# Optimization experiments

Measured on AMD Instinct MI355X. Metric: run time of the kernel, lower is better.

The kernel has to match this reference:

```python
import jax, jax.numpy as jnp
import numpy as np

HEADS = 8
DHEAD = 64
A_SCALE = 8.0  # cosine-attention logit scale (a=8 in source)
ROPE_BASE = 10000.0


def _mp_weight(w, centered):
    # Magnitude-preserving (EDM2-style) weight: optional zero-mean over fan-in,
    # unit-norm per output row, scaled by 1/sqrt(fan_in).
    if centered:
        w = w - w.mean(axis=1, keepdims=True)
    w = w / (jnp.linalg.norm(w, axis=1, keepdims=True) + 1e-8)
    return w / jnp.sqrt(jnp.asarray(w.shape[1], w.dtype))


def _rope_cos_sin(Hs, Ws, d, dtype=jnp.float32):
    # 2D axial RoPE: first d/4 rotation pairs encode row position, last d/4 column position.
    quarter = d // 4
    freqs = 1.0 / (ROPE_BASE ** (jnp.arange(quarter, dtype=dtype) / quarter))  # [d/4]
    ah = jnp.arange(Hs, dtype=dtype)[:, None] * freqs                          # [H, d/4]
    aw = jnp.arange(Ws, dtype=dtype)[:, None] * freqs                          # [W, d/4]
    ang = jnp.concatenate([
        jnp.broadcast_to(ah[:, None, :], (Hs, Ws, quarter)),
        jnp.broadcast_to(aw[None, :, :], (Hs, Ws, quarter)),
    ], axis=-1).reshape(Hs * Ws, d // 2)                                       # [L, d/2]
    return jnp.cos(ang), jnp.sin(ang)


def _apply_rope(t, cos, sin):
    # t: [N, h, L, d]; rotate interleaved pairs.
    x1, x2 = t[..., 0::2], t[..., 1::2]
    r1 = x1 * cos - x2 * sin
    r2 = x1 * sin + x2 * cos
    return jnp.stack([r1, r2], axis=-1).reshape(t.shape)


def setup_inputs() -> dict:
    key = jax.random.key(0)
    ks = jax.random.split(key, 8)
    N, C, Hs, Ws = 8, 256, 32, 32
    E, Hc = 512, 512
    return {
        "x": jax.random.normal(ks[0], (N, C, Hs, Ws), jnp.float32),
        "w": jax.random.normal(ks[1], (N, E), jnp.float32),
        "InputGain": jax.random.uniform(ks[2], (3 * Hc,), jnp.float32),
        "ResidualGain": jax.random.uniform(ks[3], (C,), jnp.float32),
        "qkv_w": jax.random.normal(ks[4], (3 * Hc, C), jnp.float32),
        "qkv_b": jnp.zeros((3 * Hc,), jnp.float32),
        "mod_w": jax.random.normal(ks[5], (E, C), jnp.float32) / jnp.sqrt(512.0),
        "proj_w": jax.random.normal(ks[6], (C, Hc), jnp.float32),
        "sinks": jnp.zeros((HEADS,), jnp.float32),
    }


def reference(x, w, InputGain, ResidualGain, qkv_w, qkv_b, mod_w, proj_w, sinks):
    N, C, Hs, Ws = x.shape
    L = Hs * Ws
    Hc = qkv_w.shape[0] // 3

    # --- fused QKV: style-modulated, biased, centered 1x1 conv with per-out-channel gain ---
    style = w @ mod_w + 1.0                                   # [N, C]
    Wq = _mp_weight(qkv_w, centered=True)                     # [3Hc, C]
    xm = x * style[:, :, None, None]
    y = jnp.einsum('nchw,oc->nohw', xm, Wq)
    y = (y + qkv_b[None, :, None, None]) * InputGain[None, :, None, None]  # [N, 3Hc, H, W]

    # --- split heads, flatten space: [N, h, L, d] ---
    y = y.reshape(N, 3, HEADS, DHEAD, L)
    q = jnp.transpose(y[:, 0], (0, 1, 3, 2))
    k = jnp.transpose(y[:, 1], (0, 1, 3, 2))
    v = jnp.transpose(y[:, 2], (0, 1, 3, 2))

    # --- 2D RoPE on q, k ---
    cos, sin = _rope_cos_sin(Hs, Ws, DHEAD, x.dtype)
    q = _apply_rope(q, cos, sin)
    k = _apply_rope(k, cos, sin)

    # --- cosine attention with per-head sink logit ---
    qn = q / (jnp.linalg.norm(q, axis=-1, keepdims=True) + 1e-8)
    kn = k / (jnp.linalg.norm(k, axis=-1, keepdims=True) + 1e-8)
    logits = A_SCALE * jnp.einsum('nhld,nhmd->nhlm', qn, kn)  # [N, h, L, L]
    sink = jnp.broadcast_to(sinks[None, :, None, None], (N, HEADS, L, 1))
    probs = jax.nn.softmax(jnp.concatenate([logits, sink], axis=-1), axis=-1)[..., :L]
    o = jnp.einsum('nhlm,nhmd->nhld', probs, v)               # [N, h, L, d]

    # --- merge heads back to map, centered 1x1 projection with per-out-channel gain ---
    o = jnp.transpose(o, (0, 1, 3, 2)).reshape(N, Hc, Hs, Ws)
    Wp = _mp_weight(proj_w, centered=True) * ResidualGain[:, None]  # [C, Hc]
    out = jnp.einsum('nchw,oc->nohw', o, Wp)
    return x + out
```

## Files before the change

### kernel.cpp

```cpp
#include <hip/hip_runtime.h>
#include <hip/hip_bf16.h>
#include <math.h>

#define NN 8
#define CC 256
#define LL 1024
#define EE 512
#define HEADS 8
#define DH 64

#define OFF_STYLE   0u
#define OFF_BIAS    2048u
#define OFF_COS     3584u
#define OFF_SIN     36352u
#define OFF_WQB     69120u
#define OFF_WPB     265728u
#define OFF_XMT     331264u
#define OFF_Q       1379840u
#define OFF_K       3476992u
#define OFF_V       5574144u
#define OFF_O       7671296u

typedef __bf16 bf16x8 __attribute__((ext_vector_type(8)));
typedef __bf16 bf16x4 __attribute__((ext_vector_type(4)));
typedef short s16x4 __attribute__((ext_vector_type(4)));
typedef short s16x8 __attribute__((ext_vector_type(8)));
typedef float f32x4 __attribute__((ext_vector_type(4)));

__global__ __launch_bounds__(256) void k_prep(
    const float* __restrict__ w, const float* __restrict__ mod_w, float* __restrict__ style,
    const float* __restrict__ qkv_w, const float* __restrict__ gain,
    const float* __restrict__ bias, __hip_bfloat16* __restrict__ wqb, float* __restrict__ biasg,
    const float* __restrict__ proj_w, const float* __restrict__ rgain,
    __hip_bfloat16* __restrict__ wpb,
    float* __restrict__ cosT, float* __restrict__ sinT) {
    int bid = blockIdx.x;
    int t = threadIdx.x;
    int wv = t >> 6, lane = t & 63;
    if (bid < 384) {
        int o = bid * 4 + wv;
        float4 v = *reinterpret_cast<const float4*>(qkv_w + o * CC + lane * 4);
        float s = v.x + v.y + v.z + v.w;
        #pragma unroll
        for (int off = 1; off < 64; off <<= 1) s += __shfl_xor(s, off);
        float mean = s * (1.0f / 256.0f);
        float c0 = v.x - mean, c1 = v.y - mean, c2 = v.z - mean, c3 = v.w - mean;
        float ss = c0 * c0 + c1 * c1 + c2 * c2 + c3 * c3;
        #pragma unroll
        for (int off = 1; off < 64; off <<= 1) ss += __shfl_xor(ss, off);
        float g = gain[o];
        float scale = g / ((sqrtf(ss) + 1e-8f) * 16.0f);
        bf16x4 outv;
        outv[0] = (__bf16)(c0 * scale); outv[1] = (__bf16)(c1 * scale);
        outv[2] = (__bf16)(c2 * scale); outv[3] = (__bf16)(c3 * scale);
        *reinterpret_cast<bf16x4*>((__bf16*)wqb + o * CC + lane * 4) = outv;
        if (lane == 0) biasg[o] = bias[o] * g;
    } else if (bid < 448) {
        int r = (bid - 384) * 4 + wv;
        const float* p = proj_w + r * 512 + lane * 8;
        float4 v0 = *reinterpret_cast<const float4*>(p);
        float4 v1 = *reinterpret_cast<const float4*>(p + 4);
        float s = v0.x + v0.y + v0.z + v0.w + v1.x + v1.y + v1.z + v1.w;
        #pragma unroll
        for (int off = 1; off < 64; off <<= 1) s += __shfl_xor(s, off);
        float mean = s * (1.0f / 512.0f);
        float c[8] = {v0.x - mean, v0.y - mean, v0.z - mean, v0.w - mean,
                      v1.x - mean, v1.y - mean, v1.z - mean, v1.w - mean};
        float ss = 0.f;
        #pragma unroll
        for (int i = 0; i < 8; ++i) ss += c[i] * c[i];
        #pragma unroll
        for (int off = 1; off < 64; off <<= 1) ss += __shfl_xor(ss, off);
        float scale = rgain[r] / ((sqrtf(ss) + 1e-8f) * 22.62741699796952f);
        bf16x8 outv;
        #pragma unroll
        for (int i = 0; i < 8; ++i) outv[i] = (__bf16)(c[i] * scale);
        *reinterpret_cast<bf16x8*>((__bf16*)wpb + r * 512 + lane * 8) = outv;
    } else if (bid < 512) {
        int idx = (bid - 448) * 256 + t;
        int l = idx >> 4, j = idx & 15;
        int hh = l >> 5, ww = l & 31;
        float f = exp2f(-(float)j * 0.8304820238941836f);
        float s1, c1, s2, c2;
        __sincosf((float)hh * f, &s1, &c1);
        __sincosf((float)ww * f, &s2, &c2);
        cosT[l * 32 + j]      = c1;
        sinT[l * 32 + j]      = s1;
        cosT[l * 32 + 16 + j] = c2;
        sinT[l * 32 + 16 + j] = s2;
    } else {
        int b = bid - 512;
        int n = b >> 2, cg = b & 3;
        int c = cg * 64 + lane;
        __shared__ float red[4][64];
        float acc = 0.f;
        #pragma unroll 8
        for (int e = wv * 128; e < wv * 128 + 128; ++e)
            acc += w[n * EE + e] * mod_w[e * CC + c];
        red[wv][lane] = acc;
        __syncthreads();
        if (wv == 0)
            style[n * CC + c] = red[0][lane] + red[1][lane] + red[2][lane] + red[3][lane] + 1.0f;
    }
}

__global__ __launch_bounds__(256) void k_xm(const float* __restrict__ x,
                                            const float* __restrict__ style,
                                            __hip_bfloat16* __restrict__ xmT) {
    int lb = blockIdx.x;
    int cb = blockIdx.y;
    int n  = blockIdx.z;
    int t = threadIdx.x;
    __shared__ float tile[64][68];
    int r = t >> 2, q = t & 3;
    float st = style[n * CC + cb * 64 + r];
    const float* xp = x + (size_t)n * (CC * LL) + (size_t)(cb * 64 + r) * LL + lb * 64 + q * 16;
    #pragma unroll
    for (int i = 0; i < 4; ++i) {
        float4 v = *reinterpret_cast<const float4*>(xp + i * 4);
        tile[r][q * 16 + i * 4 + 0] = v.x * st;
        tile[r][q * 16 + i * 4 + 1] = v.y * st;
        tile[r][q * 16 + i * 4 + 2] = v.z * st;
        tile[r][q * 16 + i * 4 + 3] = v.w * st;
    }
    __syncthreads();
    __hip_bfloat16 outv[16];
    #pragma unroll
    for (int i = 0; i < 16; ++i)
        outv[i] = __float2bfloat16(tile[q * 16 + i][r]);
    __hip_bfloat16* dst = xmT + (size_t)n * (LL * CC) + (size_t)(lb * 64 + r) * CC + cb * 64 + q * 16;
    *reinterpret_cast<bf16x8*>(dst)     = *reinterpret_cast<bf16x8*>(&outv[0]);
    *reinterpret_cast<bf16x8*>(dst + 8) = *reinterpret_cast<bf16x8*>(&outv[8]);
}

__global__ __launch_bounds__(256) void k_qkv3(const __hip_bfloat16* __restrict__ wqb,
                                              const __hip_bfloat16* __restrict__ xmT,
                                              const float* __restrict__ biasg,
                                              const float* __restrict__ cosT,
                                              const float* __restrict__ sinT,
                                              __hip_bfloat16* __restrict__ qb,
                                              __hip_bfloat16* __restrict__ kb,
                                              __hip_bfloat16* __restrict__ vt) {
    int lb = blockIdx.x;
    int ob = blockIdx.y;
    int n  = blockIdx.z;
    int tid = threadIdx.x;
    int wid = tid >> 6, lane = tid & 63;
    int wr = wid >> 1, wc = wid & 1;
    int g = lane >> 4, r16 = lane & 15;

    int o0 = ob * 128 + wr * 64;
    int l0 = lb * 128 + wc * 64;
    int part = o0 >> 9;
    int h = (o0 & 511) >> 6;

    __shared__ __hip_bfloat16 smem[32768];

    const int srow[4] = {tid >> 3, (tid + 256) >> 3, (tid + 512) >> 3, (tid + 768) >> 3};
    const int scol = (tid & 7) * 8;
    int sswz[4];
    #pragma unroll
    for (int i = 0; i < 4; ++i) sswz[i] = scol ^ ((srow[i] & 7) << 3);

    const __hip_bfloat16* Agl = wqb + (size_t)(ob * 128) * CC;
    const __hip_bfloat16* Bgl = xmT + (size_t)n * (LL * CC) + (size_t)(lb * 128) * CC;

    bf16x8 ar[4], br[4];
    #pragma unroll
    for (int i = 0; i < 4; ++i) {
        ar[i] = *reinterpret_cast<const bf16x8*>(Agl + (size_t)srow[i] * CC + scol);
        br[i] = *reinterpret_cast<const bf16x8*>(Bgl + (size_t)srow[i] * CC + scol);
    }
    #pragma unroll
    for (int i = 0; i < 4; ++i) {
        *reinterpret_cast<bf16x8*>(&smem[srow[i] * 64 + sswz[i]]) = ar[i];
        *reinterpret_cast<bf16x8*>(&smem[16384 + srow[i] * 64 + sswz[i]]) = br[i];
    }
    __syncthreads();

    f32x4 acc[4][4] = {};
    int cur = 0;
    for (int t = 0; t < 4; ++t) {
        if (t < 3) {
            int kt1 = (t + 1) * 64;
            #pragma unroll
            for (int i = 0; i < 4; ++i) {
                ar[i] = *reinterpret_cast<const bf16x8*>(Agl + (size_t)srow[i] * CC + kt1 + scol);
                br[i] = *reinterpret_cast<const bf16x8*>(Bgl + (size_t)srow[i] * CC + kt1 + scol);
            }
        }
        const __hip_bfloat16* At = &smem[cur * 8192];
        const __hip_bfloat16* Bt = &smem[16384 + cur * 8192];
        #pragma unroll
        for (int kk = 0; kk < 2; ++kk) {
            int col = (kk * 32 + g * 8) ^ ((r16 & 7) << 3);
            bf16x8 a[4], b[4];
            #pragma unroll
            for (int m = 0; m < 4; ++m)
                a[m] = *reinterpret_cast<const bf16x8*>(&At[(wr * 64 + m * 16 + r16) * 64 + col]);
            #pragma unroll
            for (int nn = 0; nn < 4; ++nn)
                b[nn] = *reinterpret_cast<const bf16x8*>(&Bt[(wc * 64 + nn * 16 + r16) * 64 + col]);
            __builtin_amdgcn_s_setprio(1);
            #pragma unroll
            for (int m = 0; m < 4; ++m)
                #pragma unroll
                for (int nn = 0; nn < 4; ++nn)
                    acc[m][nn] = __builtin_amdgcn_mfma_f32_16x16x32_bf16(a[m], b[nn], acc[m][nn], 0, 0, 0);
            __builtin_amdgcn_s_setprio(0);
        }
        if (t < 3) {
            #pragma unroll
            for (int i = 0; i < 4; ++i) {
                *reinterpret_cast<bf16x8*>(&smem[(cur ^ 1) * 8192 + srow[i] * 64 + sswz[i]]) = ar[i];
                *reinterpret_cast<bf16x8*>(&smem[16384 + (cur ^ 1) * 8192 + srow[i] * 64 + sswz[i]]) = br[i];
            }
        }
        __syncthreads();
        cur ^= 1;
    }

    __hip_bfloat16 (*sw)[64][72] = reinterpret_cast<__hip_bfloat16 (*)[64][72]>(smem);

    float bg[4][4];
    #pragma unroll
    for (int m = 0; m < 4; ++m)
        #pragma unroll
        for (int reg = 0; reg < 4; ++reg)
            bg[m][reg] = biasg[o0 + m * 16 + 4 * g + reg];

    size_t head = (size_t)(n * 8 + h);

    if (part < 2) {
        __hip_bfloat16* dst = (part == 0) ? qb : kb;
        #pragma unroll
        for (int nn = 0; nn < 4; ++nn) {
            int l = l0 + nn * 16 + r16;
            float rv[4][4];
            float ss = 0.f;
            #pragma unroll
            for (int m = 0; m < 4; ++m) {
                int j0 = m * 8 + g * 2;
                float cA = cosT[l * 32 + j0],     sA = sinT[l * 32 + j0];
                float cB = cosT[l * 32 + j0 + 1], sB = sinT[l * 32 + j0 + 1];
                float x0 = acc[m][nn][0] + bg[m][0];
                float x1 = acc[m][nn][1] + bg[m][1];
                float x2 = acc[m][nn][2] + bg[m][2];
                float x3 = acc[m][nn][3] + bg[m][3];
                rv[m][0] = x0 * cA - x1 * sA;
                rv[m][1] = x0 * sA + x1 * cA;
                rv[m][2] = x2 * cB - x3 * sB;
                rv[m][3] = x2 * sB + x3 * cB;
                ss += rv[m][0] * rv[m][0] + rv[m][1] * rv[m][1] +
                      rv[m][2] * rv[m][2] + rv[m][3] * rv[m][3];
            }
            ss += __shfl_xor(ss, 16);
            ss += __shfl_xor(ss, 32);
            float inv = 1.0f / (sqrtf(ss) + 1e-8f);
            #pragma unroll
            for (int m = 0; m < 4; ++m)
                #pragma unroll
                for (int reg = 0; reg < 4; ++reg)
                    sw[wid][nn * 16 + r16][m * 16 + 4 * g + reg] =
                        __float2bfloat16(rv[m][reg] * inv);
        }
        #pragma unroll
        for (int it = 0; it < 8; ++it) {
            int idx = lane + it * 64;
            int ll = idx >> 3, ch = idx & 7;
            bf16x8 v = *reinterpret_cast<bf16x8*>(&sw[wid][ll][ch * 8]);
            *reinterpret_cast<bf16x8*>(dst + (head * LL + l0 + ll) * DH + ch * 8) = v;
        }
    } else {
        #pragma unroll
        for (int nn = 0; nn < 4; ++nn)
            #pragma unroll
            for (int m = 0; m < 4; ++m)
                #pragma unroll
                for (int reg = 0; reg < 4; ++reg)
                    sw[wid][m * 16 + 4 * g + reg][nn * 16 + r16] =
                        __float2bfloat16(acc[m][nn][reg] + bg[m][reg]);
        #pragma unroll
        for (int it = 0; it < 8; ++it) {
            int idx = lane + it * 64;
            int dd = idx >> 3, ch = idx & 7;
            bf16x8 v = *reinterpret_cast<bf16x8*>(&sw[wid][dd][ch * 8]);
            *reinterpret_cast<bf16x8*>(vt + (head * DH + dd) * LL + l0 + ch * 8) = v;
        }
    }
}

__global__ __launch_bounds__(256) void k_attn_mfma(
    const __hip_bfloat16* __restrict__ qb, const __hip_bfloat16* __restrict__ kb,
    const __hip_bfloat16* __restrict__ vt, const float* __restrict__ sinks,
    __hip_bfloat16* __restrict__ ob) {
    int bid = blockIdx.x;
    int swz = (bid & 7) * 64 + (bid >> 3);
    int n    = swz >> 6;
    int h    = (swz >> 3) & 7;
    int qblk = swz & 7;
    int tid  = threadIdx.x;
    int wid  = tid >> 6, lane = tid & 63;
    int g = lane >> 4, r16 = lane & 15;

    size_t head = (size_t)(n * 8 + h);
    const __hip_bfloat16* Q = qb + head * (size_t)(LL * DH);
    const __hip_bfloat16* K = kb + head * (size_t)(LL * DH);
    const __hip_bfloat16* V = vt + head * (size_t)(DH * LL);
    __hip_bfloat16* O = ob + (size_t)n * (LL * 512) + h * 64;

    int q0 = qblk * 128 + wid * 32;

    __shared__ __hip_bfloat16 kls[2][64][64];
    __shared__ __hip_bfloat16 vls[2][64][64];

    const int cl0 = tid >> 3,         cd0 = (tid & 7) * 8;
    const int cl1 = (tid + 256) >> 3;
    const int ksw0 = cd0 ^ ((cl0 & 7) << 3);
    const int ksw1 = cd0 ^ ((cl1 & 7) << 3);
    const int vswA0 = cd0       ^ ((cl0 & 15) << 2);
    const int vswB0 = (cd0 + 4) ^ ((cl0 & 15) << 2);
    const int vswA1 = cd0       ^ ((cl1 & 15) << 2);
    const int vswB1 = (cd0 + 4) ^ ((cl1 & 15) << 2);

    bf16x8 qf[2][2];
    #pragma unroll
    for (int qm = 0; qm < 2; ++qm)
        #pragma unroll
        for (int dc = 0; dc < 2; ++dc)
            qf[qm][dc] = *reinterpret_cast<const bf16x8*>(
                Q + (size_t)(q0 + qm * 16 + r16) * DH + dc * 32 + g * 8);

    float snk = sinks[h];
    float m = fmaxf(8.0f, snk);
    const float c1 = 8.0f * 1.44269504f;
    const float c0 = -m * 1.44269504f;

    f32x4 oacc[2][4];
    #pragma unroll
    for (int qm = 0; qm < 2; ++qm)
        #pragma unroll
        for (int dn = 0; dn < 4; ++dn)
            oacc[qm][dn] = (f32x4){0.f, 0.f, 0.f, 0.f};
    f32x4 osum[2];
    osum[0] = (f32x4){0.f, 0.f, 0.f, 0.f};
    osum[1] = (f32x4){0.f, 0.f, 0.f, 0.f};
    const s16x4 ones = {(short)0x3F80, (short)0x3F80, (short)0x3F80, (short)0x3F80};

    bf16x8 kr0, kr1, vr0, vr1;
    kr0 = *reinterpret_cast<const bf16x8*>(K + (size_t)cl0 * DH + cd0);
    kr1 = *reinterpret_cast<const bf16x8*>(K + (size_t)cl1 * DH + cd0);
    vr0 = *reinterpret_cast<const bf16x8*>(V + (size_t)cl0 * LL + cd0);
    vr1 = *reinterpret_cast<const bf16x8*>(V + (size_t)cl1 * LL + cd0);
    {
        *reinterpret_cast<bf16x8*>(&kls[0][cl0][ksw0]) = kr0;
        *reinterpret_cast<bf16x8*>(&kls[0][cl1][ksw1]) = kr1;
        s16x8 w0 = __builtin_bit_cast(s16x8, vr0);
        s16x8 w1 = __builtin_bit_cast(s16x8, vr1);
        *reinterpret_cast<s16x4*>(&vls[0][cl0][vswA0]) = __builtin_shufflevector(w0, w0, 0, 1, 2, 3);
        *reinterpret_cast<s16x4*>(&vls[0][cl0][vswB0]) = __builtin_shufflevector(w0, w0, 4, 5, 6, 7);
        *reinterpret_cast<s16x4*>(&vls[0][cl1][vswA1]) = __builtin_shufflevector(w1, w1, 0, 1, 2, 3);
        *reinterpret_cast<s16x4*>(&vls[0][cl1][vswB1]) = __builtin_shufflevector(w1, w1, 4, 5, 6, 7);
    }
    __syncthreads();

    int cur = 0;
    for (int t = 0; t < 16; ++t) {
        if (t < 15) {
            int kt1 = t * 64 + 64;
            kr0 = *reinterpret_cast<const bf16x8*>(K + (size_t)(kt1 + cl0) * DH + cd0);
            kr1 = *reinterpret_cast<const bf16x8*>(K + (size_t)(kt1 + cl1) * DH + cd0);
            vr0 = *reinterpret_cast<const bf16x8*>(V + (size_t)cl0 * LL + kt1 + cd0);
            vr1 = *reinterpret_cast<const bf16x8*>(V + (size_t)cl1 * LL + kt1 + cd0);
        }
        f32x4 sacc[2][4];
        #pragma unroll
        for (int qm = 0; qm < 2; ++qm)
            #pragma unroll
            for (int kn = 0; kn < 4; ++kn)
                sacc[qm][kn] = (f32x4){0.f, 0.f, 0.f, 0.f};
        __builtin_amdgcn_s_setprio(1);
        #pragma unroll
        for (int kn = 0; kn < 4; ++kn) {
            #pragma unroll
            for (int dc = 0; dc < 2; ++dc) {
                bf16x8 kf = *reinterpret_cast<const bf16x8*>(
                    &kls[cur][kn * 16 + r16][(dc * 32 + g * 8) ^ ((r16 & 7) << 3)]);
                #pragma unroll
                for (int qm = 0; qm < 2; ++qm)
                    sacc[qm][kn] = __builtin_amdgcn_mfma_f32_16x16x32_bf16(
                        kf, qf[qm][dc], sacc[qm][kn], 0, 0, 0);
            }
        }
        __builtin_amdgcn_s_setprio(0);
        #pragma unroll
        for (int kn = 0; kn < 4; ++kn) {
            s16x4 pa[2];
            #pragma unroll
            for (int qm = 0; qm < 2; ++qm) {
                float p0 = exp2f(fmaf(sacc[qm][kn][0], c1, c0));
                float p1 = exp2f(fmaf(sacc[qm][kn][1], c1, c0));
                float p2 = exp2f(fmaf(sacc[qm][kn][2], c1, c0));
                float p3 = exp2f(fmaf(sacc[qm][kn][3], c1, c0));
                bf16x4 pb;
                pb[0] = (__bf16)p0; pb[1] = (__bf16)p1;
                pb[2] = (__bf16)p2; pb[3] = (__bf16)p3;
                pa[qm] = __builtin_bit_cast(s16x4, pb);
            }
            __builtin_amdgcn_s_setprio(1);
            #pragma unroll
            for (int qm = 0; qm < 2; ++qm)
                osum[qm] = __builtin_amdgcn_mfma_f32_16x16x16bf16_1k(pa[qm], ones, osum[qm], 0, 0, 0);
            #pragma unroll
            for (int dn = 0; dn < 4; ++dn) {
                s16x4 vb = *reinterpret_cast<const s16x4*>(
                    &vls[cur][dn * 16 + r16][(kn * 16 + g * 4) ^ ((r16 & 15) << 2)]);
                #pragma unroll
                for (int qm = 0; qm < 2; ++qm)
                    oacc[qm][dn] = __builtin_amdgcn_mfma_f32_16x16x16bf16_1k(
                        pa[qm], vb, oacc[qm][dn], 0, 0, 0);
            }
            __builtin_amdgcn_s_setprio(0);
        }
        if (t < 15) {
            *reinterpret_cast<bf16x8*>(&kls[cur ^ 1][cl0][ksw0]) = kr0;
            *reinterpret_cast<bf16x8*>(&kls[cur ^ 1][cl1][ksw1]) = kr1;
            s16x8 w0 = __builtin_bit_cast(s16x8, vr0);
            s16x8 w1 = __builtin_bit_cast(s16x8, vr1);
            *reinterpret_cast<s16x4*>(&vls[cur ^ 1][cl0][vswA0]) = __builtin_shufflevector(w0, w0, 0, 1, 2, 3);
            *reinterpret_cast<s16x4*>(&vls[cur ^ 1][cl0][vswB0]) = __builtin_shufflevector(w0, w0, 4, 5, 6, 7);
            *reinterpret_cast<s16x4*>(&vls[cur ^ 1][cl1][vswA1]) = __builtin_shufflevector(w1, w1, 0, 1, 2, 3);
            *reinterpret_cast<s16x4*>(&vls[cur ^ 1][cl1][vswB1]) = __builtin_shufflevector(w1, w1, 4, 5, 6, 7);
        }
        __syncthreads();
        cur ^= 1;
    }

    float sink_e = exp2f((snk - m) * 1.44269504f);
    #pragma unroll
    for (int qm = 0; qm < 2; ++qm) {
        #pragma unroll
        for (int reg = 0; reg < 4; ++reg) {
            float invq = 1.0f / (osum[qm][reg] + sink_e);
            #pragma unroll
            for (int dn = 0; dn < 4; ++dn)
                O[(size_t)(q0 + qm * 16 + 4 * g + reg) * 512 + dn * 16 + r16] =
                    __float2bfloat16(oacc[qm][dn][reg] * invq);
        }
    }
}

__global__ __launch_bounds__(256) void k_proj3(const __hip_bfloat16* __restrict__ wpb,
                                               const __hip_bfloat16* __restrict__ ob,
                                               const float* __restrict__ x,
                                               float* __restrict__ out) {
    int lb = blockIdx.x;
    int cb = blockIdx.y;
    int n  = blockIdx.z;
    int tid = threadIdx.x;
    int wid = tid >> 6, lane = tid & 63;
    int wr = wid >> 1, wc = wid & 1;
    int g = lane >> 4, r16 = lane & 15;

    int c0 = cb * 64 + wr * 32;
    int l0 = lb * 128 + wc * 64;

    __shared__ __hip_bfloat16 smem[24576];

    const int arow[2] = {tid >> 3, (tid + 256) >> 3};
    const int brow[4] = {tid >> 3, (tid + 256) >> 3, (tid + 512) >> 3, (tid + 768) >> 3};
    const int scol = (tid & 7) * 8;
    int aswz[2], bswz[4];
    #pragma unroll
    for (int i = 0; i < 2; ++i) aswz[i] = scol ^ ((arow[i] & 7) << 3);
    #pragma unroll
    for (int i = 0; i < 4; ++i) bswz[i] = scol ^ ((brow[i] & 7) << 3);

    const __hip_bfloat16* Agl = wpb + (size_t)(cb * 64) * 512;
    const __hip_bfloat16* Bgl = ob + (size_t)n * (LL * 512) + (size_t)(lb * 128) * 512;

    bf16x8 ar[2], br[4];
    #pragma unroll
    for (int i = 0; i < 2; ++i)
        ar[i] = *reinterpret_cast<const bf16x8*>(Agl + (size_t)arow[i] * 512 + scol);
    #pragma unroll
    for (int i = 0; i < 4; ++i)
        br[i] = *reinterpret_cast<const bf16x8*>(Bgl + (size_t)brow[i] * 512 + scol);
    #pragma unroll
    for (int i = 0; i < 2; ++i)
        *reinterpret_cast<bf16x8*>(&smem[arow[i] * 64 + aswz[i]]) = ar[i];
    #pragma unroll
    for (int i = 0; i < 4; ++i)
        *reinterpret_cast<bf16x8*>(&smem[8192 + brow[i] * 64 + bswz[i]]) = br[i];
    __syncthreads();

    f32x4 acc[2][4] = {};
    int cur = 0;
    for (int t = 0; t < 8; ++t) {
        if (t < 7) {
            int kt1 = (t + 1) * 64;
            #pragma unroll
            for (int i = 0; i < 2; ++i)
                ar[i] = *reinterpret_cast<const bf16x8*>(Agl + (size_t)arow[i] * 512 + kt1 + scol);
            #pragma unroll
            for (int i = 0; i < 4; ++i)
                br[i] = *reinterpret_cast<const bf16x8*>(Bgl + (size_t)brow[i] * 512 + kt1 + scol);
        }
        const __hip_bfloat16* At = &smem[cur * 4096];
        const __hip_bfloat16* Bt = &smem[8192 + cur * 8192];
        #pragma unroll
        for (int kk = 0; kk < 2; ++kk) {
            int col = (kk * 32 + g * 8) ^ ((r16 & 7) << 3);
            bf16x8 a[2], b[4];
            #pragma unroll
            for (int m = 0; m < 2; ++m)
                a[m] = *reinterpret_cast<const bf16x8*>(&At[(wr * 32 + m * 16 + r16) * 64 + col]);
            #pragma unroll
            for (int nn = 0; nn < 4; ++nn)
                b[nn] = *reinterpret_cast<const bf16x8*>(&Bt[(wc * 64 + nn * 16 + r16) * 64 + col]);
            __builtin_amdgcn_s_setprio(1);
            #pragma unroll
            for (int m = 0; m < 2; ++m)
                #pragma unroll
                for (int nn = 0; nn < 4; ++nn)
                    acc[m][nn] = __builtin_amdgcn_mfma_f32_16x16x32_bf16(a[m], b[nn], acc[m][nn], 0, 0, 0);
            __builtin_amdgcn_s_setprio(0);
        }
        if (t < 7) {
            #pragma unroll
            for (int i = 0; i < 2; ++i)
                *reinterpret_cast<bf16x8*>(&smem[(cur ^ 1) * 4096 + arow[i] * 64 + aswz[i]]) = ar[i];
            #pragma unroll
            for (int i = 0; i < 4; ++i)
                *reinterpret_cast<bf16x8*>(&smem[8192 + (cur ^ 1) * 8192 + brow[i] * 64 + bswz[i]]) = br[i];
        }
        __syncthreads();
        cur ^= 1;
    }

    #pragma unroll
    for (int m = 0; m < 2; ++m) {
        #pragma unroll
        for (int reg = 0; reg < 4; ++reg) {
            int c = c0 + m * 16 + 4 * g + reg;
            #pragma unroll
            for (int nn = 0; nn < 4; ++nn) {
                int l = l0 + nn * 16 + r16;
                size_t idx = (size_t)n * (CC * LL) + (size_t)c * LL + l;
                out[idx] = x[idx] + acc[m][nn][reg];
            }
        }
    }
}

extern "C" void kernel_launch(void* const* d_in, const int* in_sizes, int n_in,
                              void* d_out, int out_size, void* d_ws, size_t ws_size,
                              hipStream_t stream) {
    const float* x       = (const float*)d_in[0];
    const float* w       = (const float*)d_in[1];
    const float* igain   = (const float*)d_in[2];
    const float* rgain   = (const float*)d_in[3];
    const float* qkv_w   = (const float*)d_in[4];
    const float* qkv_b   = (const float*)d_in[5];
    const float* mod_w   = (const float*)d_in[6];
    const float* proj_w  = (const float*)d_in[7];
    const float* sinks   = (const float*)d_in[8];
    float* out = (float*)d_out;
    float* ws  = (float*)d_ws;

    float* style = ws + OFF_STYLE;
    float* biasg = ws + OFF_BIAS;
    float* cosT  = ws + OFF_COS;
    float* sinT  = ws + OFF_SIN;
    __hip_bfloat16* wqb = (__hip_bfloat16*)(ws + OFF_WQB);
    __hip_bfloat16* wpb = (__hip_bfloat16*)(ws + OFF_WPB);
    __hip_bfloat16* xmT = (__hip_bfloat16*)(ws + OFF_XMT);
    __hip_bfloat16* qb  = (__hip_bfloat16*)(ws + OFF_Q);
    __hip_bfloat16* kb  = (__hip_bfloat16*)(ws + OFF_K);
    __hip_bfloat16* vt  = (__hip_bfloat16*)(ws + OFF_V);
    __hip_bfloat16* obuf = (__hip_bfloat16*)(ws + OFF_O);

    k_prep<<<544, 256, 0, stream>>>(w, mod_w, style, qkv_w, igain, qkv_b, wqb, biasg,
                                    proj_w, rgain, wpb, cosT, sinT);
    k_xm<<<dim3(16, 4, NN), 256, 0, stream>>>(x, style, xmT);
    k_qkv3<<<dim3(8, 12, NN), 256, 0, stream>>>(wqb, xmT, biasg, cosT, sinT, qb, kb, vt);
    k_attn_mfma<<<512, 256, 0, stream>>>(qb, kb, vt, sinks, obuf);
    k_proj3<<<dim3(8, 4, NN), 256, 0, stream>>>(wpb, obuf, x, out);
}
```

Before: 83.63 us.

## Fold softmax scale into Q and widen attention K/V tiles to 128

The cosine-attention logit scale (8·log2e) is folded into the Q normalization in the QKV kernel, so the attention loop feeds raw scores straight into exp2f. This drops the fixed max-subtraction, which is safe because scores are bounded, and the sink term is adjusted to match. The attention kernel now stages 128-key K/V tiles per iteration (8 iterations instead of 16), halving barriers and global-load rounds. The cost is double the shared memory per block and more staging registers, which may lower occupancy.

Result: faster. 81.91 us (-2.1%).

```diff
diff --git a/kernel.cpp b/kernel.cpp
--- a/kernel.cpp
+++ b/kernel.cpp
@@ -233,6 +233,7 @@
 
     if (part < 2) {
         __hip_bfloat16* dst = (part == 0) ? qb : kb;
+        float qscale = (part == 0) ? 11.541560327111707f : 1.0f;
         #pragma unroll
         for (int nn = 0; nn < 4; ++nn) {
             int l = l0 + nn * 16 + r16;
@@ -256,7 +257,7 @@
             }
             ss += __shfl_xor(ss, 16);
             ss += __shfl_xor(ss, 32);
-            float inv = 1.0f / (sqrtf(ss) + 1e-8f);
+            float inv = qscale / (sqrtf(ss) + 1e-8f);
             #pragma unroll
             for (int m = 0; m < 4; ++m)
                 #pragma unroll
@@ -311,17 +312,18 @@
 
     int q0 = qblk * 128 + wid * 32;
 
-    __shared__ __hip_bfloat16 kls[2][64][64];
-    __shared__ __hip_bfloat16 vls[2][64][64];
-
-    const int cl0 = tid >> 3,         cd0 = (tid & 7) * 8;
-    const int cl1 = (tid + 256) >> 3;
-    const int ksw0 = cd0 ^ ((cl0 & 7) << 3);
-    const int ksw1 = cd0 ^ ((cl1 & 7) << 3);
-    const int vswA0 = cd0       ^ ((cl0 & 15) << 2);
-    const int vswB0 = (cd0 + 4) ^ ((cl0 & 15) << 2);
-    const int vswA1 = cd0       ^ ((cl1 & 15) << 2);
-    const int vswB1 = (cd0 + 4) ^ ((cl1 & 15) << 2);
+    __shared__ __hip_bfloat16 kls[2][128][64];
+    __shared__ __hip_bfloat16 vls[2][64][128];
+
+    const int kcl = tid >> 3, kcd = (tid & 7) * 8;
+    const int vcl = tid >> 4, vcd = (tid & 15) * 8;
+    int kswz[4], vswzA[4], vswzB[4];
+    #pragma unroll
+    for (int i = 0; i < 4; ++i) {
+        kswz[i]  = kcd ^ (((kcl + i * 32) & 7) << 3);
+        vswzA[i] = vcd ^ (((vcl + i * 16) & 15) << 2);
+        vswzB[i] = (vcd + 4) ^ (((vcl + i * 16) & 15) << 2);
+    }
 
     bf16x8 qf[2][2];
     #pragma unroll
@@ -332,9 +334,6 @@
                 Q + (size_t)(q0 + qm * 16 + r16) * DH + dc * 32 + g * 8);
 
     float snk = sinks[h];
-    float m = fmaxf(8.0f, snk);
-    const float c1 = 8.0f * 1.44269504f;
-    const float c0 = -m * 1.44269504f;
 
     f32x4 oacc[2][4];
     #pragma unroll
@@ -347,96 +346,99 @@
     osum[1] = (f32x4){0.f, 0.f, 0.f, 0.f};
     const s16x4 ones = {(short)0x3F80, (short)0x3F80, (short)0x3F80, (short)0x3F80};
 
-    bf16x8 kr0, kr1, vr0, vr1;
-    kr0 = *reinterpret_cast<const bf16x8*>(K + (size_t)cl0 * DH + cd0);
-    kr1 = *reinterpret_cast<const bf16x8*>(K + (size_t)cl1 * DH + cd0);
-    vr0 = *reinterpret_cast<const bf16x8*>(V + (size_t)cl0 * LL + cd0);
-    vr1 = *reinterpret_cast<const bf16x8*>(V + (size_t)cl1 * LL + cd0);
-    {
-        *reinterpret_cast<bf16x8*>(&kls[0][cl0][ksw0]) = kr0;
-        *reinterpret_cast<bf16x8*>(&kls[0][cl1][ksw1]) = kr1;
-        s16x8 w0 = __builtin_bit_cast(s16x8, vr0);
-        s16x8 w1 = __builtin_bit_cast(s16x8, vr1);
-        *reinterpret_cast<s16x4*>(&vls[0][cl0][vswA0]) = __builtin_shufflevector(w0, w0, 0, 1, 2, 3);
-        *reinterpret_cast<s16x4*>(&vls[0][cl0][vswB0]) = __builtin_shufflevector(w0, w0, 4, 5, 6, 7);
-        *reinterpret_cast<s16x4*>(&vls[0][cl1][vswA1]) = __builtin_shufflevector(w1, w1, 0, 1, 2, 3);
-        *reinterpret_cast<s16x4*>(&vls[0][cl1][vswB1]) = __builtin_shufflevector(w1, w1, 4, 5, 6, 7);
+    bf16x8 kr[4], vr[4];
+    #pragma unroll
+    for (int i = 0; i < 4; ++i) {
+        kr[i] = *reinterpret_cast<const bf16x8*>(K + (size_t)(kcl + i * 32) * DH + kcd);
+        vr[i] = *reinterpret_cast<const bf16x8*>(V + (size_t)(vcl + i * 16) * LL + vcd);
+    }
+    #pragma unroll
+    for (int i = 0; i < 4; ++i) {
+        *reinterpret_cast<bf16x8*>(&kls[0][kcl + i * 32][kswz[i]]) = kr[i];
+        s16x8 wv8 = __builtin_bit_cast(s16x8, vr[i]);
+        *reinterpret_cast<s16x4*>(&vls[0][vcl + i * 16][vswzA[i]]) = __builtin_shufflevector(wv8, wv8, 0, 1, 2, 3);
+        *reinterpret_cast<s16x4*>(&vls[0][vcl + i * 16][vswzB[i]]) = __builtin_shufflevector(wv8, wv8, 4, 5, 6, 7);
     }
     __syncthreads();
 
     int cur = 0;
-    for (int t = 0; t < 16; ++t) {
-        if (t < 15) {
-            int kt1 = t * 64 + 64;
-            kr0 = *reinterpret_cast<const bf16x8*>(K + (size_t)(kt1 + cl0) * DH + cd0);
-            kr1 = *reinterpret_cast<const bf16x8*>(K + (size_t)(kt1 + cl1) * DH + cd0);
-            vr0 = *reinterpret_cast<const bf16x8*>(V + (size_t)cl0 * LL + kt1 + cd0);
-            vr1 = *reinterpret_cast<const bf16x8*>(V + (size_t)cl1 * LL + kt1 + cd0);
-        }
-        f32x4 sacc[2][4];
-        #pragma unroll
-        for (int qm = 0; qm < 2; ++qm)
-            #pragma unroll
-            for (int kn = 0; kn < 4; ++kn)
-                sacc[qm][kn] = (f32x4){0.f, 0.f, 0.f, 0.f};
-        __builtin_amdgcn_s_setprio(1);
-        #pragma unroll
-        for (int kn = 0; kn < 4; ++kn) {
-            #pragma unroll
-            for (int dc = 0; dc < 2; ++dc) {
-                bf16x8 kf = *reinterpret_cast<const bf16x8*>(
-                    &kls[cur][kn * 16 + r16][(dc * 32 + g * 8) ^ ((r16 & 7) << 3)]);
+    for (int t = 0; t < 8; ++t) {
+        if (t < 7) {
+            int kt1 = (t + 1) * 128;
+            #pragma unroll
+            for (int i = 0; i < 4; ++i) {
+                kr[i] = *reinterpret_cast<const bf16x8*>(K + (size_t)(kt1 + kcl + i * 32) * DH + kcd);
+                vr[i] = *reinterpret_cast<const bf16x8*>(V + (size_t)(vcl + i * 16) * LL + kt1 + vcd);
+            }
+        }
+        #pragma unroll
+        for (int sub = 0; sub < 2; ++sub) {
+            f32x4 sacc[2][4];
+            #pragma unroll
+            for (int qm = 0; qm < 2; ++qm)
+                #pragma unroll
+                for (int kn = 0; kn < 4; ++kn)
+                    sacc[qm][kn] = (f32x4){0.f, 0.f, 0.f, 0.f};
+            __builtin_amdgcn_s_setprio(1);
+            #pragma unroll
+            for (int kn = 0; kn < 4; ++kn) {
+                int krow = sub * 64 + kn * 16 + r16;
+                #pragma unroll
+                for (int dc = 0; dc < 2; ++dc) {
+                    bf16x8 kf = *reinterpret_cast<const bf16x8*>(
+                        &kls[cur][krow][(dc * 32 + g * 8) ^ ((r16 & 7) << 3)]);
+                    #pragma unroll
+                    for (int qm = 0; qm < 2; ++qm)
+                        sacc[qm][kn] = __builtin_amdgcn_mfma_f32_16x16x32_bf16(
+                            kf, qf[qm][dc], sacc[qm][kn], 0, 0, 0);
+                }
+            }
+            __builtin_amdgcn_s_setprio(0);
+            #pragma unroll
+            for (int kn = 0; kn < 4; ++kn) {
+                s16x4 pa[2];
+                #pragma unroll
+                for (int qm = 0; qm < 2; ++qm) {
+                    float p0 = exp2f(sacc[qm][kn][0]);
+                    float p1 = exp2f(sacc[qm][kn][1]);
+                    float p2 = exp2f(sacc[qm][kn][2]);
+                    float p3 = exp2f(sacc[qm][kn][3]);
+                    bf16x4 pb;
+                    pb[0] = (__bf16)p0; pb[1] = (__bf16)p1;
+                    pb[2] = (__bf16)p2; pb[3] = (__bf16)p3;
+                    pa[qm] = __builtin_bit_cast(s16x4, pb);
+                }
+                __builtin_amdgcn_s_setprio(1);
                 #pragma unroll
                 for (int qm = 0; qm < 2; ++qm)
-                    sacc[qm][kn] = __builtin_amdgcn_mfma_f32_16x16x32_bf16(
-                        kf, qf[qm][dc], sacc[qm][kn], 0, 0, 0);
-            }
-        }
-        __builtin_amdgcn_s_setprio(0);
-        #pragma unroll
-        for (int kn = 0; kn < 4; ++kn) {
-            s16x4 pa[2];
-            #pragma unroll
-            for (int qm = 0; qm < 2; ++qm) {
-                float p0 = exp2f(fmaf(sacc[qm][kn][0], c1, c0));
-                float p1 = exp2f(fmaf(sacc[qm][kn][1], c1, c0));
-                float p2 = exp2f(fmaf(sacc[qm][kn][2], c1, c0));
-                float p3 = exp2f(fmaf(sacc[qm][kn][3], c1, c0));
-                bf16x4 pb;
-                pb[0] = (__bf16)p0; pb[1] = (__bf16)p1;
-                pb[2] = (__bf16)p2; pb[3] = (__bf16)p3;
-                pa[qm] = __builtin_bit_cast(s16x4, pb);
-            }
-            __builtin_amdgcn_s_setprio(1);
-            #pragma unroll
-            for (int qm = 0; qm < 2; ++qm)
-                osum[qm] = __builtin_amdgcn_mfma_f32_16x16x16bf16_1k(pa[qm], ones, osum[qm], 0, 0, 0);
-            #pragma unroll
-            for (int dn = 0; dn < 4; ++dn) {
-                s16x4 vb = *reinterpret_cast<const s16x4*>(
-                    &vls[cur][dn * 16 + r16][(kn * 16 + g * 4) ^ ((r16 & 15) << 2)]);
-                #pragma unroll
-                for (int qm = 0; qm < 2; ++qm)
-                    oacc[qm][dn] = __builtin_amdgcn_mfma_f32_16x16x16bf16_1k(
-                        pa[qm], vb, oacc[qm][dn], 0, 0, 0);
-            }
-            __builtin_amdgcn_s_setprio(0);
-        }
-        if (t < 15) {
-            *reinterpret_cast<bf16x8*>(&kls[cur ^ 1][cl0][ksw0]) = kr0;
-            *reinterpret_cast<bf16x8*>(&kls[cur ^ 1][cl1][ksw1]) = kr1;
-            s16x8 w0 = __builtin_bit_cast(s16x8, vr0);
-            s16x8 w1 = __builtin_bit_cast(s16x8, vr1);
-            *reinterpret_cast<s16x4*>(&vls[cur ^ 1][cl0][vswA0]) = __builtin_shufflevector(w0, w0, 0, 1, 2, 3);
-            *reinterpret_cast<s16x4*>(&vls[cur ^ 1][cl0][vswB0]) = __builtin_shufflevector(w0, w0, 4, 5, 6, 7);
-            *reinterpret_cast<s16x4*>(&vls[cur ^ 1][cl1][vswA1]) = __builtin_shufflevector(w1, w1, 0, 1, 2, 3);
-            *reinterpret_cast<s16x4*>(&vls[cur ^ 1][cl1][vswB1]) = __builtin_shufflevector(w1, w1, 4, 5, 6, 7);
+                    osum[qm] = __builtin_amdgcn_mfma_f32_16x16x16bf16_1k(pa[qm], ones, osum[qm], 0, 0, 0);
+                #pragma unroll
+                for (int dn = 0; dn < 4; ++dn) {
+                    int vcol = sub * 64 + kn * 16 + g * 4;
+                    s16x4 vb = *reinterpret_cast<const s16x4*>(
+                        &vls[cur][dn * 16 + r16][vcol ^ ((r16 & 15) << 2)]);
+                    #pragma unroll
+                    for (int qm = 0; qm < 2; ++qm)
+                        oacc[qm][dn] = __builtin_amdgcn_mfma_f32_16x16x16bf16_1k(
+                            pa[qm], vb, oacc[qm][dn], 0, 0, 0);
+                }
+                __builtin_amdgcn_s_setprio(0);
+            }
+        }
+        if (t < 7) {
+            #pragma unroll
+            for (int i = 0; i < 4; ++i) {
+                *reinterpret_cast<bf16x8*>(&kls[cur ^ 1][kcl + i * 32][kswz[i]]) = kr[i];
+                s16x8 wv8 = __builtin_bit_cast(s16x8, vr[i]);
+                *reinterpret_cast<s16x4*>(&vls[cur ^ 1][vcl + i * 16][vswzA[i]]) = __builtin_shufflevector(wv8, wv8, 0, 1, 2, 3);
+                *reinterpret_cast<s16x4*>(&vls[cur ^ 1][vcl + i * 16][vswzB[i]]) = __builtin_shufflevector(wv8, wv8, 4, 5, 6, 7);
+            }
         }
         __syncthreads();
         cur ^= 1;
     }
 
-    float sink_e = exp2f((snk - m) * 1.44269504f);
+    float sink_e = exp2f(snk * 1.44269504f);
     #pragma unroll
     for (int qm = 0; qm < 2; ++qm) {
         #pragma unroll
```
